# Optimization experiments

Measured on AMD Instinct MI355X. Metric: run time of the kernel, lower is better.

The kernel has to match this reference:

```python
import jax, jax.numpy as jnp
import numpy as np

T = 2048          # total (flattened) tokens
HID = 4096
NQ = 32           # query heads
NKV = 8           # kv heads
D = 128           # head_dim
B = 4             # dllm block length (block-sparse attention block)
WIN = 1024        # sliding window
EPS = 1e-6


def _rope_tables():
    # standard RoPE cos/sin tables, half-dim frequencies duplicated
    inv_freq = 1.0 / (10000.0 ** (np.arange(0, D, 2, dtype=np.float32) / D))
    pos = np.arange(T, dtype=np.float32)
    freqs = np.outer(pos, inv_freq)                     # [T, D/2]
    emb = np.concatenate([freqs, freqs], axis=-1)       # [T, D]
    return jnp.asarray(np.cos(emb)), jnp.asarray(np.sin(emb))


def setup_inputs() -> dict:
    key = jax.random.key(0)
    ks = jax.random.split(key, 4)
    cos, sin = _rope_tables()
    return {
        "hidden_states": jax.random.normal(ks[0], (T, HID), jnp.float32),
        "cos": cos,
        "sin": sin,
        "w_qkv": jax.random.normal(ks[1], (HID, (NQ + 2 * NKV) * D), jnp.float32) * (HID ** -0.5),
        "q_norm_w": jnp.ones((D,), jnp.float32),
        "k_norm_w": jnp.ones((D,), jnp.float32),
        "w_o": jax.random.normal(ks[2], (NQ * D, HID), jnp.float32) * ((NQ * D) ** -0.5),
    }


def _rmsnorm(x, w):
    # per-head RMSNorm over last dim (head_dim)
    var = jnp.mean(jnp.square(x), axis=-1, keepdims=True)
    return x * jax.lax.rsqrt(var + EPS) * w


def _rotate_half(x):
    x1, x2 = jnp.split(x, 2, axis=-1)
    return jnp.concatenate([-x2, x1], axis=-1)


def reference(hidden_states, cos, sin, w_qkv, q_norm_w, k_norm_w, w_o):
    # fused QKV projection on flattened tokens [T, HID]
    qkv = hidden_states @ w_qkv                                  # [T, (NQ+2NKV)*D]
    q, k, v = jnp.split(qkv, [NQ * D, (NQ + NKV) * D], axis=-1)
    q = q.reshape(T, NQ, D)
    k = k.reshape(T, NKV, D)
    v = v.reshape(T, NKV, D)

    # per-head QK RMSNorm
    q = _rmsnorm(q, q_norm_w)
    k = _rmsnorm(k, k_norm_w)

    # RoPE
    c = cos[:, None, :]
    s = sin[:, None, :]
    q = q * c + _rotate_half(q) * s
    k = k * c + _rotate_half(k) * s

    # GQA: expand kv heads to query heads
    groups = NQ // NKV
    k = jnp.repeat(k, groups, axis=1)                            # [T, NQ, D]
    v = jnp.repeat(v, groups, axis=1)

    # block-sparse (dLLM block-causal) + sliding-window mask:
    # token q attends to token j iff block(j) <= block(q) (full bidirectional
    # attention within a dllm block, causal across blocks) AND j is within
    # the sliding window.
    pos = jnp.arange(T)
    qb = pos // B
    allowed = (qb[None, :] <= qb[:, None]) & ((pos[:, None] - pos[None, :]) < WIN)

    scale = D ** -0.5
    scores = jnp.einsum("qhd,khd->hqk", q, k) * scale            # [NQ, T, T]
    scores = jnp.where(allowed[None, :, :], scores, jnp.float32(-1e30))
    probs = jax.nn.softmax(scores, axis=-1)
    attn = jnp.einsum("hqk,khd->qhd", probs, v)                   # [T, NQ, D]

    out = attn.reshape(T, NQ * D) @ w_o                           # [T, HID]
    return out
```

## Files before the change

### kernel.cpp

```cpp
#include <hip/hip_runtime.h>
#include <hip/hip_bf16.h>

typedef unsigned short u16;
typedef __attribute__((ext_vector_type(8))) short bf16x8;
typedef __attribute__((ext_vector_type(4))) float f32x4;
typedef __attribute__((ext_vector_type(8))) u16 u16x8;
typedef __attribute__((ext_vector_type(4))) u16 u16x4;

#define T_SEQ 2048
#define HID 4096
#define NQ 32
#define NKV 8
#define DH 128
#define WIN 1024

__device__ __forceinline__ u16 f2bf(float f) {
  union { float f; unsigned int u; } v; v.f = f;
  unsigned int u = v.u;
  unsigned int r = (u + 0x7FFFu + ((u >> 16) & 1u)) >> 16;
  return (u16)r;
}
__device__ __forceinline__ float bf2f(u16 b) {
  union { unsigned int u; float f; } v; v.u = ((unsigned int)b) << 16;
  return v.f;
}

__device__ __forceinline__ void gload16(const void* g, void* l) {
  __builtin_amdgcn_global_load_lds(
      (const __attribute__((address_space(1))) unsigned int*)g,
      (__attribute__((address_space(3))) unsigned int*)l, 16, 0, 0);
}

__global__ __launch_bounds__(256) void f32_to_bf16(const float* __restrict__ in,
                                                   u16* __restrict__ out, int n) {
  int i = (blockIdx.x * 256 + threadIdx.x) * 8;
  if (i >= n) return;
  float4 a = *(const float4*)(in + i);
  float4 b = *(const float4*)(in + i + 4);
  u16x8 r;
  r[0] = f2bf(a.x); r[1] = f2bf(a.y); r[2] = f2bf(a.z); r[3] = f2bf(a.w);
  r[4] = f2bf(b.x); r[5] = f2bf(b.y); r[6] = f2bf(b.z); r[7] = f2bf(b.w);
  *(u16x8*)(out + i) = r;
}

__global__ __launch_bounds__(256) void transpose_f32_to_bf16(const float* __restrict__ in,
                                                             u16* __restrict__ out,
                                                             int R, int C) {
  __shared__ float tile[32][33];
  int c0 = blockIdx.x * 32, r0 = blockIdx.y * 32;
  int tx = threadIdx.x, ty = threadIdx.y;
  for (int i = 0; i < 32; i += 8)
    tile[ty + i][tx] = in[(size_t)(r0 + ty + i) * C + c0 + tx];
  __syncthreads();
  for (int i = 0; i < 32; i += 8)
    out[(size_t)(c0 + ty + i) * R + r0 + tx] = f2bf(tile[tx][ty + i]);
}

template <int NF, bool BF16OUT>
__global__ __launch_bounds__(512, 2) void gemm_np(const u16* __restrict__ A,
                                                  const u16* __restrict__ Bt,
                                                  void* __restrict__ Cv,
                                                  int N, int K, int NT) {
  constexpr int HN = NF * 16;
  constexpr int BN = 4 * HN;
  constexpr int NB = BN / 64;
  __shared__ u16 lsA[2][16384];
  __shared__ u16 lsB[2][BN * 64];
  const int tid = threadIdx.x;
  const int lane = tid & 63, w = tid >> 6;
  const int wm = w >> 1, wn = w & 1;
  const int l15 = lane & 15, l4 = lane >> 4;

  const int nwg = gridDim.x;
  const int cpx = nwg >> 3;
  const int bid = blockIdx.x;
  const int swz = (bid & 7) * cpx + (bid >> 3);
  const int bm = (swz & 7) * 256;
  const int bn = (swz >> 3) * BN;

  auto stageA = [&](int unit, int slot, int kt) {
    int r = tid >> 3, cp = tid & 7;
    int scp = cp ^ (r & 7);
    gload16(A + (size_t)(bm + unit * 64 + r) * K + kt * 64 + scp * 8,
            (char*)lsA[slot] + (unit * 512 + tid) * 16);
  };
  auto stageB = [&](int unit, int slot, int kt) {
    int r = tid >> 3, cp = tid & 7;
    int scp = cp ^ (r & 7);
    gload16(Bt + (size_t)(bn + unit * 64 + r) * K + kt * 64 + scp * 8,
            (char*)lsB[slot] + (unit * 512 + tid) * 16);
  };
  auto rdA = [&](int slot, int mh, int mf, int ks) -> bf16x8 {
    int r = wm * 64 + mh * 32 + mf * 16 + l15;
    int ch = (ks * 4 + l4) ^ (r & 7);
    return *(const bf16x8*)(lsA[slot] + r * 64 + ch * 8);
  };
  auto rdB = [&](int slot, int nh, int nf, int ks) -> bf16x8 {
    int r = wn * 2 * HN + nh * HN + nf * 16 + l15;
    int ch = (ks * 4 + l4) ^ (r & 7);
    return *(const bf16x8*)(lsB[slot] + r * 64 + ch * 8);
  };

#define WAIT_NB() do { if constexpr (NB == 3) asm volatile("s_waitcnt vmcnt(3)" ::: "memory"); \
                       else                   asm volatile("s_waitcnt vmcnt(2)" ::: "memory"); } while (0)

  f32x4 acc[4][2 * NF] = {};
  bf16x8 afA[2][2], afB[2][2], bfr0[NF][2], bfr1[NF][2];

  stageA(0, 0, 0); stageA(1, 0, 0); stageA(2, 0, 0); stageA(3, 0, 0);
#pragma unroll
  for (int u = 0; u < NB; ++u) stageB(u, 0, 0);
#pragma unroll
  for (int u = 0; u < NB; ++u) stageB(u, 1, 1);
  WAIT_NB();
  __builtin_amdgcn_s_barrier();

  for (int t = 0; t < NT; ++t) {
    const int s = t & 1;
    const int ktA = (t + 1 < NT) ? t + 1 : NT - 1;
    const int ktB = (t + 2 < NT) ? t + 2 : NT - 1;

#pragma unroll
    for (int mf = 0; mf < 2; ++mf)
#pragma unroll
      for (int ks = 0; ks < 2; ++ks) afA[mf][ks] = rdA(s, 0, mf, ks);
#pragma unroll
    for (int nf = 0; nf < NF; ++nf)
#pragma unroll
      for (int ks = 0; ks < 2; ++ks) bfr0[nf][ks] = rdB(s, 0, nf, ks);
    stageA(0, s ^ 1, ktA); stageA(1, s ^ 1, ktA);
    __builtin_amdgcn_s_barrier();
    asm volatile("s_waitcnt lgkmcnt(0)" ::: "memory");
    __builtin_amdgcn_sched_barrier(0);
    __builtin_amdgcn_s_setprio(1);
#pragma unroll
    for (int mf = 0; mf < 2; ++mf)
#pragma unroll
      for (int nf = 0; nf < NF; ++nf) {
        acc[mf][nf] = __builtin_amdgcn_mfma_f32_16x16x32_bf16(afA[mf][0], bfr0[nf][0], acc[mf][nf], 0, 0, 0);
        acc[mf][nf] = __builtin_amdgcn_mfma_f32_16x16x32_bf16(afA[mf][1], bfr0[nf][1], acc[mf][nf], 0, 0, 0);
      }
    __builtin_amdgcn_s_setprio(0);
    __builtin_amdgcn_s_barrier();

#pragma unroll
    for (int nf = 0; nf < NF; ++nf)
#pragma unroll
      for (int ks = 0; ks < 2; ++ks) bfr1[nf][ks] = rdB(s, 1, nf, ks);
    stageA(2, s ^ 1, ktA); stageA(3, s ^ 1, ktA);
    __builtin_amdgcn_s_barrier();
    asm volatile("s_waitcnt lgkmcnt(0)" ::: "memory");
    __builtin_amdgcn_sched_barrier(0);
    __builtin_amdgcn_s_setprio(1);
#pragma unroll
    for (int mf = 0; mf < 2; ++mf)
#pragma unroll
      for (int nf = 0; nf < NF; ++nf) {
        acc[mf][NF + nf] = __builtin_amdgcn_mfma_f32_16x16x32_bf16(afA[mf][0], bfr1[nf][0], acc[mf][NF + nf], 0, 0, 0);
        acc[mf][NF + nf] = __builtin_amdgcn_mfma_f32_16x16x32_bf16(afA[mf][1], bfr1[nf][1], acc[mf][NF + nf], 0, 0, 0);
      }
    __builtin_amdgcn_s_setprio(0);
    __builtin_amdgcn_s_barrier();

#pragma unroll
    for (int mf = 0; mf < 2; ++mf)
#pragma unroll
      for (int ks = 0; ks < 2; ++ks) afB[mf][ks] = rdA(s, 1, mf, ks);
#pragma unroll
    for (int u = 0; u < NB - 1; ++u) stageB(u, s, ktB);
    __builtin_amdgcn_s_barrier();
    asm volatile("s_waitcnt lgkmcnt(0)" ::: "memory");
    __builtin_amdgcn_sched_barrier(0);
    __builtin_amdgcn_s_setprio(1);
#pragma unroll
    for (int mf = 0; mf < 2; ++mf)
#pragma unroll
      for (int nf = 0; nf < NF; ++nf) {
        acc[2 + mf][nf] = __builtin_amdgcn_mfma_f32_16x16x32_bf16(afB[mf][0], bfr0[nf][0], acc[2 + mf][nf], 0, 0, 0);
        acc[2 + mf][nf] = __builtin_amdgcn_mfma_f32_16x16x32_bf16(afB[mf][1], bfr0[nf][1], acc[2 + mf][nf], 0, 0, 0);
      }
    __builtin_amdgcn_s_setprio(0);
    __builtin_amdgcn_s_barrier();

    stageB(NB - 1, s, ktB);
    __builtin_amdgcn_s_barrier();
    __builtin_amdgcn_s_setprio(1);
#pragma unroll
    for (int mf = 0; mf < 2; ++mf)
#pragma unroll
      for (int nf = 0; nf < NF; ++nf) {
        acc[2 + mf][NF + nf] = __builtin_amdgcn_mfma_f32_16x16x32_bf16(afB[mf][0], bfr1[nf][0], acc[2 + mf][NF + nf], 0, 0, 0);
        acc[2 + mf][NF + nf] = __builtin_amdgcn_mfma_f32_16x16x32_bf16(afB[mf][1], bfr1[nf][1], acc[2 + mf][NF + nf], 0, 0, 0);
      }
    __builtin_amdgcn_s_setprio(0);
    WAIT_NB();
    __builtin_amdgcn_s_barrier();
  }

  asm volatile("s_waitcnt vmcnt(0)" ::: "memory");

#pragma unroll
  for (int mi = 0; mi < 4; ++mi)
#pragma unroll
    for (int ni = 0; ni < 2 * NF; ++ni) {
      int row = bm + wm * 64 + mi * 16 + l4 * 4;
      int col = bn + wn * 2 * HN + ni * 16 + l15;
      if constexpr (BF16OUT) {
        u16* dst = (u16*)Cv;
#pragma unroll
        for (int j = 0; j < 4; ++j)
          dst[(size_t)(row + j) * N + col] = f2bf(acc[mi][ni][j]);
      } else {
        float* p = (float*)Cv + (size_t)row * N + col;
        p[0] = acc[mi][ni][0];
        p[(size_t)N] = acc[mi][ni][1];
        p[2 * (size_t)N] = acc[mi][ni][2];
        p[3 * (size_t)N] = acc[mi][ni][3];
      }
    }
#undef WAIT_NB
}

__global__ __launch_bounds__(256) void rope_kernel(const u16* __restrict__ qkv,
                                                   const float* __restrict__ cosb,
                                                   const float* __restrict__ sinb,
                                                   const float* __restrict__ qw,
                                                   const float* __restrict__ kw,
                                                   u16* __restrict__ Qo,
                                                   u16* __restrict__ Ko,
                                                   u16* __restrict__ Vt) {
  int wid = threadIdx.x >> 6, lane = threadIdx.x & 63;
  int item = blockIdx.x * 4 + wid;
  int t = item / 48, hid = item % 48;
  const u16* x = qkv + (size_t)t * 6144 + hid * 128;
  float x1 = bf2f(x[lane]), x2 = bf2f(x[lane + 64]);
  if (hid < NQ + NKV) {
    float ss = x1 * x1 + x2 * x2;
    for (int off = 32; off; off >>= 1) ss += __shfl_xor(ss, off);
    float inv = rsqrtf(ss * (1.0f / 128.0f) + 1e-6f);
    const float* wn = (hid < NQ) ? qw : kw;
    float n1 = x1 * inv * wn[lane], n2 = x2 * inv * wn[lane + 64];
    float c1 = cosb[t * 128 + lane], s1 = sinb[t * 128 + lane];
    float c2 = cosb[t * 128 + lane + 64], s2 = sinb[t * 128 + lane + 64];
    float o1 = n1 * c1 - n2 * s1;
    float o2 = n2 * c2 + n1 * s2;
    if (hid < NQ) {
      const float scale = 0.08838834764831845f;
      u16* q = Qo + ((size_t)hid * T_SEQ + t) * 128;
      q[lane] = f2bf(o1 * scale); q[lane + 64] = f2bf(o2 * scale);
    } else {
      int h = hid - NQ;
      u16* k = Ko + ((size_t)h * T_SEQ + t) * 128;
      k[lane] = f2bf(o1); k[lane + 64] = f2bf(o2);
    }
  } else {
    int h = hid - (NQ + NKV);
    Vt[((size_t)h * 128 + lane) * T_SEQ + t] = x[lane];
    Vt[((size_t)h * 128 + lane + 64) * T_SEQ + t] = x[lane + 64];
  }
}

__global__ __launch_bounds__(256) void attn_kernel(const u16* __restrict__ Q,
                                                   const u16* __restrict__ Kb,
                                                   const u16* __restrict__ Vt,
                                                   u16* __restrict__ O) {
  __shared__ u16 kls[2][64 * 128];
  __shared__ u16 vls[2][128 * 64];
  __shared__ u16 plds[4][16 * 72];

  const int tid = threadIdx.x;
  const int lane = tid & 63, w = tid >> 6;
  const int l15 = lane & 15, l4 = lane >> 4;
  const int h = blockIdx.x;
  const int q0 = blockIdx.y * 64;
  const int wq0 = q0 + w * 16;
  const int kvh = h >> 2;

  bf16x8 qf[4];
  {
    const u16* qrow = Q + ((size_t)h * T_SEQ + (wq0 + l15)) * DH;
    for (int ks = 0; ks < 4; ++ks)
      qf[ks] = *(const bf16x8*)(qrow + ks * 32 + l4 * 8);
  }

  f32x4 acc[8] = {};
  float m = -1e30f, lsum = 0.f;

  int ks0 = q0 - (WIN - 1); if (ks0 < 0) ks0 = 0;
  ks0 &= ~63;
  const int kend = q0;

  auto stage = [&](int b, int k0) {
#pragma unroll
    for (int c = 0; c < 4; ++c) {
      int base = w * 4096 + c * 1024;
      int idx = base / 16 + lane;
      {
        int row = idx >> 4;
        int col = (idx & 15) ^ (row & 7);
        gload16(Kb + ((size_t)kvh * T_SEQ + k0 + row) * DH + col * 8,
                (char*)kls[b] + base);
      }
      {
        int d = idx >> 3;
        int ch = (idx & 7) ^ (d & 7);
        gload16(Vt + ((size_t)kvh * DH + d) * T_SEQ + k0 + ch * 8,
                (char*)vls[b] + base);
      }
    }
  };

  stage(0, ks0);
  int buf = 0;
  for (int k0 = ks0; k0 <= kend; k0 += 64) {
    bool more = (k0 + 64 <= kend);
    if (more) stage(buf ^ 1, k0 + 64);
    if (more) { asm volatile("s_waitcnt vmcnt(8)" ::: "memory"); }
    else      { asm volatile("s_waitcnt vmcnt(0)" ::: "memory"); }
    __builtin_amdgcn_s_barrier();
    __builtin_amdgcn_sched_barrier(0);

    if (k0 <= wq0 + 15 && k0 + 63 >= wq0 - (WIN - 1)) {
      f32x4 st[4];
#pragma unroll
      for (int kh = 0; kh < 4; ++kh) {
        f32x4 s = {};
        int row = kh * 16 + l15;
        const char* kb = (const char*)kls[buf] + row * 256;
#pragma unroll
        for (int ks = 0; ks < 4; ++ks) {
          int chunk = (ks * 4 + l4) ^ (row & 7);
          bf16x8 kf = *(const bf16x8*)(kb + chunk * 16);
          s = __builtin_amdgcn_mfma_f32_16x16x32_bf16(kf, qf[ks], s, 0, 0, 0);
        }
        st[kh] = s;
      }
      const int q = wq0 + l15;
      float pv[4][4];
      float mx = -3e38f;
#pragma unroll
      for (int kh = 0; kh < 4; ++kh)
#pragma unroll
        for (int i = 0; i < 4; ++i) {
          int k = k0 + kh * 16 + l4 * 4 + i;
          bool ok = ((k >> 2) <= (q >> 2)) && (q - k < WIN);
          float s = ok ? st[kh][i] : -3e38f;
          pv[kh][i] = s;
          mx = fmaxf(mx, s);
        }
      mx = fmaxf(mx, __shfl_xor(mx, 16));
      mx = fmaxf(mx, __shfl_xor(mx, 32));
      if (!__all(mx <= m + 8.f)) {
        float mn = fmaxf(m, mx);
        float sc = __expf(m - mn);
        m = mn;
        lsum *= sc;
#pragma unroll
        for (int nt = 0; nt < 8; ++nt)
#pragma unroll
          for (int i = 0; i < 4; ++i) acc[nt][i] *= sc;
      }
      float rs = 0.f;
#pragma unroll
      for (int kh = 0; kh < 4; ++kh)
#pragma unroll
        for (int i = 0; i < 4; ++i) {
          float p = __expf(pv[kh][i] - m);
          pv[kh][i] = p;
          rs += p;
        }
      rs += __shfl_xor(rs, 16);
      rs += __shfl_xor(rs, 32);
      lsum += rs;
      u16* pw = plds[w];
#pragma unroll
      for (int kh = 0; kh < 4; ++kh) {
        unsigned int d0 = (unsigned int)f2bf(pv[kh][0]) | ((unsigned int)f2bf(pv[kh][1]) << 16);
        unsigned int d1 = (unsigned int)f2bf(pv[kh][2]) | ((unsigned int)f2bf(pv[kh][3]) << 16);
        *(unsigned int*)(pw + l15 * 72 + kh * 16 + l4 * 4) = d0;
        *(unsigned int*)(pw + l15 * 72 + kh * 16 + l4 * 4 + 2) = d1;
      }
      bf16x8 pf0 = *(const bf16x8*)(pw + l15 * 72 + l4 * 8);
      bf16x8 pf1 = *(const bf16x8*)(pw + l15 * 72 + 32 + l4 * 8);
#pragma unroll
      for (int nt = 0; nt < 8; ++nt) {
        int d = nt * 16 + l15;
        int ch0 = l4 ^ (d & 7);
        int ch1 = (4 + l4) ^ (d & 7);
        bf16x8 vf0 = *(const bf16x8*)((const char*)vls[buf] + d * 128 + ch0 * 16);
        bf16x8 vf1 = *(const bf16x8*)((const char*)vls[buf] + d * 128 + ch1 * 16);
        acc[nt] = __builtin_amdgcn_mfma_f32_16x16x32_bf16(vf0, pf0, acc[nt], 0, 0, 0);
        acc[nt] = __builtin_amdgcn_mfma_f32_16x16x32_bf16(vf1, pf1, acc[nt], 0, 0, 0);
      }
    }
    __builtin_amdgcn_sched_barrier(0);
    __builtin_amdgcn_s_barrier();
    buf ^= 1;
  }

  float inv = 1.0f / lsum;
#pragma unroll
  for (int nt = 0; nt < 8; ++nt) {
    u16x4 o;
#pragma unroll
    for (int i = 0; i < 4; ++i) o[i] = f2bf(acc[nt][i] * inv);
    *(u16x4*)(O + (size_t)(wq0 + l15) * (NQ * DH) + h * DH + nt * 16 + l4 * 4) = o;
  }
}

extern "C" void kernel_launch(void* const* d_in, const int* in_sizes, int n_in,
                              void* d_out, int out_size, void* d_ws, size_t ws_size,
                              hipStream_t stream) {
  const float* hidden = (const float*)d_in[0];
  const float* cosb   = (const float*)d_in[1];
  const float* sinb   = (const float*)d_in[2];
  const float* w_qkv  = (const float*)d_in[3];
  const float* qnw    = (const float*)d_in[4];
  const float* knw    = (const float*)d_in[5];
  const float* w_o    = (const float*)d_in[6];
  float* out = (float*)d_out;
  char* ws = (char*)d_ws;

  u16*   wqkvT  = (u16*)(ws);
  u16*   hid_bf = (u16*)(ws + ((size_t)48 << 20));
  u16*   qkv_bf = (u16*)(ws + ((size_t)64 << 20));
  u16*   q_bf   = (u16*)(ws + ((size_t)112 << 20));
  u16*   k_bf   = (u16*)(ws + ((size_t)128 << 20));
  u16*   vt_bf  = (u16*)(ws + ((size_t)132 << 20));
  u16*   attn_bf= (u16*)(ws + ((size_t)48 << 20));
  u16*   woT    = (u16*)(ws);

  f32_to_bf16<<<4096, 256, 0, stream>>>(hidden, hid_bf, T_SEQ * HID);
  transpose_f32_to_bf16<<<dim3(192, 128), dim3(32, 8), 0, stream>>>(w_qkv, wqkvT, HID, 6144);
  gemm_np<3, true><<<256, 512, 0, stream>>>(hid_bf, wqkvT, qkv_bf, 6144, HID, 64);
  transpose_f32_to_bf16<<<dim3(128, 128), dim3(32, 8), 0, stream>>>(w_o, woT, NQ * DH, HID);
  rope_kernel<<<(T_SEQ * 48) / 4, 256, 0, stream>>>(qkv_bf, cosb, sinb, qnw, knw, q_bf, k_bf, vt_bf);
  attn_kernel<<<dim3(NQ, T_SEQ / 64), 256, 0, stream>>>(q_bf, k_bf, vt_bf, attn_bf);
  gemm_np<2, false><<<256, 512, 0, stream>>>(attn_bf, woT, out, HID, NQ * DH, 64);
}
```

Before: 338.7 us.

## Vectorize weight transpose, skip masking on interior tiles, add MFMA priority hints

The weight transpose kernel now uses 64x64 tiles, loads four floats per thread as float4 and writes four bf16 values per store. This cuts the number of memory transactions for the per-call weight conversion. The attention kernel skips per-element mask computation when a 64-key tile lies entirely inside the allowed region, and raises wave priority around the MFMA sections with s_setprio. Risks include LDS bank conflicts from the strided tile reads in the transposed store loop, and an interior-tile bound that must exactly match the window and block-causal rules.

```diff
diff --git a/kernel.cpp b/kernel.cpp
--- a/kernel.cpp
+++ b/kernel.cpp
@@ -46,14 +46,25 @@
 __global__ __launch_bounds__(256) void transpose_f32_to_bf16(const float* __restrict__ in,
                                                              u16* __restrict__ out,
                                                              int R, int C) {
-  __shared__ float tile[32][33];
-  int c0 = blockIdx.x * 32, r0 = blockIdx.y * 32;
+  __shared__ float tile[64][65];
+  int c0 = blockIdx.x * 64, r0 = blockIdx.y * 64;
   int tx = threadIdx.x, ty = threadIdx.y;
-  for (int i = 0; i < 32; i += 8)
-    tile[ty + i][tx] = in[(size_t)(r0 + ty + i) * C + c0 + tx];
+#pragma unroll
+  for (int i = 0; i < 64; i += 16) {
+    float4 v = *(const float4*)(in + (size_t)(r0 + ty + i) * C + c0 + tx * 4);
+    tile[ty + i][tx * 4 + 0] = v.x;
+    tile[ty + i][tx * 4 + 1] = v.y;
+    tile[ty + i][tx * 4 + 2] = v.z;
+    tile[ty + i][tx * 4 + 3] = v.w;
+  }
   __syncthreads();
-  for (int i = 0; i < 32; i += 8)
-    out[(size_t)(c0 + ty + i) * R + r0 + tx] = f2bf(tile[tx][ty + i]);
+#pragma unroll
+  for (int i = 0; i < 64; i += 16) {
+    u16x4 o;
+#pragma unroll
+    for (int j = 0; j < 4; ++j) o[j] = f2bf(tile[tx * 4 + j][ty + i]);
+    *(u16x4*)(out + (size_t)(c0 + ty + i) * R + r0 + tx * 4) = o;
+  }
 }
 
 template <int NF, bool BF16OUT>
@@ -322,6 +333,7 @@
 
     if (k0 <= wq0 + 15 && k0 + 63 >= wq0 - (WIN - 1)) {
       f32x4 st[4];
+      __builtin_amdgcn_s_setprio(1);
 #pragma unroll
       for (int kh = 0; kh < 4; ++kh) {
         f32x4 s = {};
@@ -335,19 +347,30 @@
         }
         st[kh] = s;
       }
+      __builtin_amdgcn_s_setprio(0);
       const int q = wq0 + l15;
       float pv[4][4];
       float mx = -3e38f;
-#pragma unroll
-      for (int kh = 0; kh < 4; ++kh)
-#pragma unroll
-        for (int i = 0; i < 4; ++i) {
-          int k = k0 + kh * 16 + l4 * 4 + i;
-          bool ok = ((k >> 2) <= (q >> 2)) && (q - k < WIN);
-          float s = ok ? st[kh][i] : -3e38f;
-          pv[kh][i] = s;
-          mx = fmaxf(mx, s);
-        }
+      if (k0 + 64 <= wq0 && k0 >= wq0 - 1008) {
+#pragma unroll
+        for (int kh = 0; kh < 4; ++kh)
+#pragma unroll
+          for (int i = 0; i < 4; ++i) {
+            pv[kh][i] = st[kh][i];
+            mx = fmaxf(mx, pv[kh][i]);
+          }
+      } else {
+#pragma unroll
+        for (int kh = 0; kh < 4; ++kh)
+#pragma unroll
+          for (int i = 0; i < 4; ++i) {
+            int k = k0 + kh * 16 + l4 * 4 + i;
+            bool ok = ((k >> 2) <= (q >> 2)) && (q - k < WIN);
+            float s = ok ? st[kh][i] : -3e38f;
+            pv[kh][i] = s;
+            mx = fmaxf(mx, s);
+          }
+      }
       mx = fmaxf(mx, __shfl_xor(mx, 16));
       mx = fmaxf(mx, __shfl_xor(mx, 32));
       if (!__all(mx <= m + 8.f)) {
@@ -382,6 +405,7 @@
       }
       bf16x8 pf0 = *(const bf16x8*)(pw + l15 * 72 + l4 * 8);
       bf16x8 pf1 = *(const bf16x8*)(pw + l15 * 72 + 32 + l4 * 8);
+      __builtin_amdgcn_s_setprio(1);
 #pragma unroll
       for (int nt = 0; nt < 8; ++nt) {
         int d = nt * 16 + l15;
@@ -392,6 +416,7 @@
         acc[nt] = __builtin_amdgcn_mfma_f32_16x16x32_bf16(vf0, pf0, acc[nt], 0, 0, 0);
         acc[nt] = __builtin_amdgcn_mfma_f32_16x16x32_bf16(vf1, pf1, acc[nt], 0, 0, 0);
       }
+      __builtin_amdgcn_s_setprio(0);
     }
     __builtin_amdgcn_sched_barrier(0);
     __builtin_amdgcn_s_barrier();
@@ -431,9 +456,9 @@
   u16*   woT    = (u16*)(ws);
 
   f32_to_bf16<<<4096, 256, 0, stream>>>(hidden, hid_bf, T_SEQ * HID);
-  transpose_f32_to_bf16<<<dim3(192, 128), dim3(32, 8), 0, stream>>>(w_qkv, wqkvT, HID, 6144);
+  transpose_f32_to_bf16<<<dim3(96, 64), dim3(16, 16), 0, stream>>>(w_qkv, wqkvT, HID, 6144);
   gemm_np<3, true><<<256, 512, 0, stream>>>(hid_bf, wqkvT, qkv_bf, 6144, HID, 64);
-  transpose_f32_to_bf16<<<dim3(128, 128), dim3(32, 8), 0, stream>>>(w_o, woT, NQ * DH, HID);
+  transpose_f32_to_bf16<<<dim3(64, 64), dim3(16, 16), 0, stream>>>(w_o, woT, NQ * DH, HID);
   rope_kernel<<<(T_SEQ * 48) / 4, 256, 0, stream>>>(qkv_bf, cosb, sinb, qnw, knw, q_bf, k_bf, vt_bf);
   attn_kernel<<<dim3(NQ, T_SEQ / 64), 256, 0, stream>>>(q_bf, k_bf, vt_bf, attn_bf);
   gemm_np<2, false><<<256, 512, 0, stream>>>(attn_bf, woT, out, HID, NQ * DH, 64);
```

After: 330.2 us. -2.5%, faster.
